# Kernel optimization log

Measured on AMD Instinct MI355X. Metric: run time of the kernel, lower is better.

## Reference

```python
import jax, jax.numpy as jnp
import numpy as np

_S = np.float32(1.0 / np.sqrt(2.0))
_lo = np.array([_S, _S], np.float32)   # dec_lo reversed == rec_lo for db1
_hi = np.array([_S, -_S], np.float32)  # dec_hi reversed == rec_hi for db1
# filters[k][i,j]: k=0 LL/2, k=1 hi(i)*lo(j), k=2 lo(i)*hi(j), k=3 hi*hi  (matches torch unsqueeze outer products)
DEC = np.stack([np.outer(_lo, _lo) / 2.0, np.outer(_hi, _lo), np.outer(_lo, _hi), np.outer(_hi, _hi)]).astype(np.float32)
INV = np.stack([np.outer(_lo, _lo) * 2.0, np.outer(_hi, _lo), np.outer(_lo, _hi), np.outer(_hi, _hi)]).astype(np.float32)
INV_FLIP = np.ascontiguousarray(INV[:, ::-1, ::-1])  # spatially flipped for conv_transpose-as-dilated-conv

DN = ('NCHW', 'OIHW', 'NCHW')


def wt(x):
    # single grouped (depthwise x4) strided conv == per-channel loop in the original
    N, C, H, W = x.shape
    k = jnp.broadcast_to(jnp.asarray(DEC)[None], (C, 4, 2, 2)).reshape(C * 4, 1, 2, 2)
    r = jax.lax.conv_general_dilated(x, k, (2, 2), 'VALID', dimension_numbers=DN, feature_group_count=C)
    r = r.reshape(N, C, 4, H // 2, W // 2)
    r = jnp.concatenate([r[:, :, :1], (r[:, :, 1:] + 1.0) / 2.0], axis=2)  # detail remap
    return r.reshape(N, 4 * C, H // 2, W // 2)


def iwt(v):
    N, C4, H, W = v.shape
    C = C4 // 4
    r = v.reshape(N, C, 4, H, W)
    r = jnp.concatenate([r[:, :, :1], 2.0 * r[:, :, 1:] - 1.0], axis=2).reshape(N, C4, H, W)
    k = jnp.broadcast_to(jnp.asarray(INV_FLIP)[None], (C, 4, 2, 2))
    # conv_transpose2d(stride=2, k=2) == dilated conv with lhs_dilation=2, pad 1, flipped kernel
    return jax.lax.conv_general_dilated(r, k, (1, 1), ((1, 1), (1, 1)), lhs_dilation=(2, 2),
                                        dimension_numbers=DN, feature_group_count=C)


def ws_conv(x, w, b, pad):
    # weight standardization: subtract mean over (in,kh,kw), divide by per-filter std (unbiased) + 1e-5
    wc = w - w.mean(axis=(1, 2, 3), keepdims=True)
    std = wc.reshape(w.shape[0], -1).std(axis=1, ddof=1).reshape(-1, 1, 1, 1) + 1e-5
    y = jax.lax.conv_general_dilated(x, wc / std, (1, 1), ((pad, pad), (pad, pad)), dimension_numbers=DN)
    return y if b is None else y + b[None, :, None, None]


def gn(x, g, b, G):
    N, C, H, W = x.shape
    xr = x.reshape(N, G, -1)
    m = xr.mean(-1, keepdims=True)
    v = xr.var(-1, keepdims=True)
    xr = (xr - m) * jax.lax.rsqrt(v + 1e-5)
    return xr.reshape(N, C, H, W) * g[None, :, None, None] + b[None, :, None, None]


def lrelu(t):
    return jnp.where(t > 0, t, 0.2 * t)


def setup_inputs() -> dict:
    key = jax.random.key(0)
    ks = iter(jax.random.split(key, 32))
    f32 = jnp.float32
    d = {}
    d['x'] = jax.random.normal(next(ks), (16, 3, 256, 256), f32)
    def wgt(shape):
        return 0.05 * jax.random.normal(next(ks), shape, f32)
    def bias(n):
        return 0.01 * jax.random.normal(next(ks), (n,), f32)
    c = 16
    d['conv1_w'], d['conv1_b'] = wgt((c, 12, 3, 3)), bias(c)
    d['conv2_w'], d['conv2_b'] = wgt((4 * c, 4 * c, 3, 3)), bias(4 * c)
    d['conv3_w'], d['conv3_b'] = wgt((16 * c, 16 * c, 3, 3)), bias(16 * c)
    d['conv4_w'], d['conv4_b'] = wgt((64 * c, 64 * c, 3, 3)), bias(64 * c)
    d['convd1_w'], d['convd1_b'] = wgt((12, c, 3, 3)), bias(12)
    d['convd2_w'], d['convd2_b'] = wgt((c, 2 * c, 3, 3)), bias(c)
    d['convd3_w'], d['convd3_b'] = wgt((4 * c, 8 * c, 3, 3)), bias(4 * c)
    d['convd4_w'], d['convd4_b'] = wgt((16 * c, 32 * c, 3, 3)), bias(16 * c)
    d['final_w'] = wgt((2, 3, 1, 1))
    for name, n in (('gn1', c), ('gn2', 4 * c), ('gn3', 16 * c), ('gn4', 64 * c)):
        d[name + '_w'] = 1.0 + 0.1 * jax.random.normal(next(ks), (n,), f32)
        d[name + '_b'] = 0.01 * jax.random.normal(next(ks), (n,), f32)
    return d


def reference(x, conv1_w, conv1_b, conv2_w, conv2_b, conv3_w, conv3_b, conv4_w, conv4_b,
              convd1_w, convd1_b, convd2_w, convd2_b, convd3_w, convd3_b, convd4_w, convd4_b,
              final_w, gn1_w, gn1_b, gn2_w, gn2_b, gn3_w, gn3_b, gn4_w, gn4_b):
    w1 = wt(x)
    c1 = gn(lrelu(ws_conv(w1, conv1_w, conv1_b, 1)), gn1_w, gn1_b, 2)
    w2 = wt(c1)
    c2 = gn(lrelu(ws_conv(w2, conv2_w, conv2_b, 1)), gn2_w, gn2_b, 8)
    w3 = wt(c2)
    c3 = gn(lrelu(ws_conv(w3, conv3_w, conv3_b, 1)), gn3_w, gn3_b, 32)
    w4 = wt(c3)
    c4 = gn(lrelu(ws_conv(w4, conv4_w, conv4_b, 1)), gn4_w, gn4_b, 128)
    c5 = gn(lrelu(ws_conv(c4, conv4_w, conv4_b, 1)), gn4_w, gn4_b, 128)
    c6 = ws_conv(c5, conv4_w, conv4_b, 1)
    ic4 = lrelu(c6 + w4)
    iw4 = jnp.concatenate([c3, iwt(ic4)], axis=1)
    ic3 = gn(lrelu(ws_conv(iw4, convd4_w, convd4_b, 1)), gn3_w, gn3_b, 32)
    iw3 = jnp.concatenate([c2, iwt(ic3)], axis=1)
    ic2 = gn(lrelu(ws_conv(iw3, convd3_w, convd3_b, 1)), gn2_w, gn2_b, 8)
    iw2 = jnp.concatenate([c1, iwt(ic2)], axis=1)
    ic1 = gn(lrelu(ws_conv(iw2, convd2_w, convd2_b, 1)), gn1_w, gn1_b, 2)
    iw1 = lrelu(ws_conv(ic1, convd1_w, convd1_b, 1))
    y = ws_conv(iwt(iw1), final_w, None, 0)
    return y
```

## Files before the change

kernel.cpp:

```cpp
#include <hip/hip_runtime.h>
#include <math.h>


#define NB 16

typedef _Float16 f16;
typedef _Float16 f16x8 __attribute__((ext_vector_type(8)));
typedef _Float16 f16x4 __attribute__((ext_vector_type(4)));
typedef float f32x4 __attribute__((ext_vector_type(4)));
typedef float f32x2 __attribute__((ext_vector_type(2)));
typedef unsigned int u32;

#define LLDS16(gp, lp)                                                          \
  __builtin_amdgcn_global_load_lds((const __attribute__((address_space(1))) u32*)(const void*)(gp), \
                                   (__attribute__((address_space(3))) u32*)(void*)(lp), 16, 0, 0)

__device__ __forceinline__ void ws_reduce(const float* wp, int fan, float* red,
                                          float& mean, float& inv) {
  float s = 0.f, s2 = 0.f;
  for (int i = threadIdx.x; i < fan; i += 256) { float v = wp[i]; s += v; s2 += v * v; }
  red[threadIdx.x] = s; red[256 + threadIdx.x] = s2;
  __syncthreads();
  for (int st = 128; st > 0; st >>= 1) {
    if (threadIdx.x < st) {
// ... 58 lines not shown

__global__ void halo2_kernel(f16* b0, int c0, int h0, int w0, int n0,
                             f16* b1, int c1, int h1, int w1, int total) {
  int idx = blockIdx.x * 256 + threadIdx.x;
  if (idx >= total) return;
  if (idx < n0) halo_write(b0, c0, h0, w0, idx);
  else halo_write(b1, c1, h1, w1, idx - n0);
}

__global__ void zero_halo_kernel(f16* __restrict__ buf, int C, int H, int W, int total8) {
  int idx = blockIdx.x * 256 + threadIdx.x;
  if (idx >= total8) return;
  halo_write(buf, C, H, W, idx);
}

__global__ void wt_kernel(const float* __restrict__ in, float* __restrict__ out,
                          int C, int Ho, int Wo, int total) {
  int idx = blockIdx.x * 256 + threadIdx.x;
  if (idx >= total) return;
  int w = idx % Wo; int t = idx / Wo;
  int h = t % Ho; t /= Ho;
  int c = t % C; int n = t / C;
  int Wi = 2 * Wo;
  const float* ip = in + (((size_t)n * C + c) * (2 * Ho) + 2 * h) * Wi + 2 * w;
  float a = ip[0], b = ip[1], cc = ip[Wi], d = ip[Wi + 1];
  size_t cs = (size_t)Ho * Wo;
  float* op = out + (((size_t)n * 4 * C + 4 * c) * Ho + h) * Wo + w;
  op[0]      = 0.25f * (a + b + cc + d);
  op[cs]     = 0.25f * (a + b - cc - d) + 0.5f;
  op[2 * cs] = 0.25f * (a - b + cc - d) + 0.5f;
  op[3 * cs] = 0.25f * (a - b - cc + d) + 0.5f;
}

__global__ __launch_bounds__(256) void wt_nhwc_kernel(
    const float* __restrict__ in, f16* __restrict__ out, float* __restrict__ out32,
    int C, int Ho, int Wo) {
  __shared__ f16 sm[32][264];
  int HWo = Ho * Wo;
  int p0 = blockIdx.x * 256, c0 = blockIdx.y * 8, n = blockIdx.z;
  int t = threadIdx.x;
  int p = p0 + t; int h = p / Wo; int ww = p - h * Wo;
  int Wi = 2 * Wo;
  int C4 = 4 * C;
#pragma unroll
  for (int r = 0; r < 8; ++r) {
    const float* ip = in + (((size_t)n * C + c0 + r) * (2 * Ho) + 2 * h) * Wi + 2 * ww;
    f32x2 u0 = *(const f32x2*)ip;
    f32x2 u1 = *(const f32x2*)(ip + Wi);
    float a = u0.x, b = u0.y, cc = u1.x, d = u1.y;
    float v0 = 0.25f * (a + b + cc + d);
    float v1 = 0.25f * (a + b - cc - d) + 0.5f;
    float v2 = 0.25f * (a - b + cc - d) + 0.5f;
    float v3 = 0.25f * (a - b - cc + d) + 0.5f;
    sm[4 * r][t]     = (f16)v0;
    sm[4 * r + 1][t] = (f16)v1;
    sm[4 * r + 2][t] = (f16)v2;
    sm[4 * r + 3][t] = (f16)v3;
    if (out32) {
      float* op = out32 + (((size_t)n * C4 + 4 * (c0 + r)) * Ho + h) * Wo + ww;
      size_t cs = (size_t)HWo;
      op[0] = v0; op[cs] = v1; op[2 * cs] = v2; op[3 * cs] = v3;
    }
  }
  __syncthreads();
#pragma unroll
  for (int i = 0; i < 4; ++i) {
    int c = t + i * 256;
    int pl = c >> 2, cio = (c & 3) * 8;
    f16x8 v;
#pragma unroll
    for (int u = 0; u < 8; ++u) v[u] = sm[cio + u][pl];
    int pp = p0 + pl; int y = pp / Wo; int x = pp - y * Wo;
    *(f16x8*)(out + (((size_t)n * (Ho + 2) + y + 1) * (Wo + 2) + x + 1) * C4 + c0 * 4 + cio) = v;
  }
}

__global__ void concat_iwt_kernel(const float* __restrict__ skip, const float* __restrict__ v,
                                  float* __restrict__ out, const float* __restrict__ gnp,
                                  const float* __restrict__ gamma, const float* __restrict__ beta,
                                  int G, int Sg, int len, int C, int Hh, int Wh,
                                  int totalA, int total) {
  int idx = blockIdx.x * 256 + threadIdx.x;
// ... 62 lines not shown
    f16* __restrict__ out, int C, int H, int W, int G, int Sg, int len) {
  __shared__ f16 sm[32][264];
  int HW = H * W;
  int p0 = blockIdx.x * 256, c0 = blockIdx.y * 32, n = blockIdx.z;
  int t = threadIdx.x;
  int cpg = C / G;
  const float* ip = in + ((size_t)n * C + c0) * HW + p0;
#pragma unroll 8
  for (int r = 0; r < 32; ++r) {
    int c = c0 + r; int g = c / cpg;
    const float* pp = gnp + (size_t)((n * G + g) * Sg) * 2;
    float s = 0.f, s2 = 0.f;
    for (int i = 0; i < Sg; ++i) { s += pp[2 * i]; s2 += pp[2 * i + 1]; }
    float mean = s / (float)len;
    float var = s2 / (float)len - mean * mean;
    if (var < 0.f) var = 0.f;
    float inv = rsqrtf(var + 1e-5f);
    float ga = gamma[c], be = beta[c];
    sm[r][t] = (f16)((ip[(size_t)r * HW + t] - mean) * inv * ga + be);
  }
  __syncthreads();
#pragma unroll
  for (int i = 0; i < 4; ++i) {
    int c = t + i * 256;
    int pl = c >> 2, cio = (c & 3) * 8;
    f16x8 v;
#pragma unroll
    for (int u = 0; u < 8; ++u) v[u] = sm[cio + u][pl];
    int p = p0 + pl; int y = p / W; int x = p - y * W;
    *(f16x8*)(out + (((size_t)n * (H + 2) + y + 1) * (W + 2) + x + 1) * C + c0 + cio) = v;
  }
}

__global__ __launch_bounds__(256) void conv_mfma6_kernel(
    const f16* __restrict__ A, const f16* __restrict__ Wp,
    f16* __restrict__ part, int Cin, int H, int W, int Cout, int HW) {
  constexpr int CH = 128 * 64;
  __shared__ f16 Asm[2 * CH];
  __shared__ f16 Bsm[2 * CH];

  const int tid = threadIdx.x;
  const int w = tid >> 6, lane = tid & 63;
  const int m0 = blockIdx.x * 128;
  const int co0 = blockIdx.y * 128;
  const int Wp2 = W + 2;

  const f16* gA[4]; const f16* gB[4];
  int lOff[4];
#pragma unroll
  for (int e = 0; e < 4; ++e) {
    int c = e * 256 + tid;
    int r = c >> 3, j = c & 7;
    int jx = j ^ (r & 7);
    int m = m0 + r; int n = m / HW; int p = m - n * HW;
    int y = p / W; int x = p - y * W;
    gA[e] = A + (((size_t)n * (H + 2) + y + 1) * Wp2 + (x + 1)) * Cin + jx * 8;
    gB[e] = Wp + (size_t)(co0 + r) * Cin + jx * 8;
    lOff[e] = (e * 256 + w * 64) * 8;
  }

  const int wm = w & 1, wn = w >> 1;
  const int lr = lane & 15, quad = lane >> 4;
  int aoffs[4][2], boffs[4][2];
#pragma unroll
  for (int i = 0; i < 4; ++i)
#pragma unroll
    for (int kk = 0; kk < 2; ++kk) {
      int r = wm * 64 + i * 16 + lr;
      int cidx = kk * 4 + quad;
      aoffs[i][kk] = (r * 8 + (cidx ^ (r & 7))) * 8;
      int rb = wn * 64 + i * 16 + lr;
      boffs[i][kk] = (rb * 8 + (cidx ^ (rb & 7))) * 8;
    }

  f32x4 acc[4][4];
#pragma unroll
  for (int i = 0; i < 4; ++i)
#pragma unroll
    for (int j = 0; j < 4; ++j) acc[i][j] = (f32x4){0.f, 0.f, 0.f, 0.f};

  const int kpt = Cin >> 6;
  const int nit = (9 * kpt) / gridDim.z;
  const int it0 = blockIdx.z * nit;
  const size_t bstride = (size_t)Cout * Cin;

  auto stageAB = [&](int it, int sel) {
    int tap = it / kpt, kk = it - tap * kpt;
    int dy = tap / 3 - 1, dx = tap % 3 - 1;
    long offA = ((long)dy * Wp2 + dx) * Cin + (kk << 6);
    long offB = (long)tap * bstride + (kk << 6);
    f16* ab = Asm + sel * CH;
    f16* bb = Bsm + sel * CH;
#pragma unroll
    for (int e = 0; e < 4; ++e) {
      LLDS16(gA[e] + offA, ab + lOff[e]);
      LLDS16(gB[e] + offB, bb + lOff[e]);
    }
  };

  stageAB(it0, 0);
  int sel = 0;
  for (int ii = 0; ii < nit; ++ii) {
    __syncthreads();
    if (ii + 1 < nit) stageAB(it0 + ii + 1, sel ^ 1);
    const f16* ab = Asm + sel * CH;
    const f16* bb = Bsm + sel * CH;
    f16x8 af[4][2], bf[4][2];
#pragma unroll
    for (int i = 0; i < 4; ++i)
#pragma unroll
      for (int kk = 0; kk < 2; ++kk) {
        af[i][kk] = *(const f16x8*)&ab[aoffs[i][kk]];
        bf[i][kk] = *(const f16x8*)&bb[boffs[i][kk]];
      }
#pragma unroll
    for (int kk = 0; kk < 2; ++kk)
#pragma unroll
      for (int i = 0; i < 4; ++i)
#pragma unroll
        for (int j = 0; j < 4; ++j)
          acc[i][j] = __builtin_amdgcn_mfma_f32_16x16x32_f16(af[i][kk], bf[j][kk], acc[i][j], 0, 0, 0);
    sel ^= 1;
  }

  const size_t pbase = (size_t)blockIdx.z * NB * Cout * HW;
#pragma unroll
  for (int i = 0; i < 4; ++i) {
    int mg = m0 + wm * 64 + i * 16 + quad * 4;
    int n = mg / HW, p = mg - n * HW;
#pragma unroll
    for (int j = 0; j < 4; ++j) {
      int co = co0 + wn * 64 + j * 16 + lr;
      f32x4 v = acc[i][j];
      f16x4 h;
#pragma unroll
      for (int r = 0; r < 4; ++r) h[r] = (f16)v[r];
      *(f16x4*)&part[pbase + ((size_t)n * Cout + co) * HW + p] = h;
    }
  }
}

__global__ __launch_bounds__(256) void reduceS_kernel(
    const f16* __restrict__ part, const float* __restrict__ bias,
    const float* __restrict__ add, float* __restrict__ out,
    int Cout, int HW, int S, int do_lrelu, int total4,
    float* __restrict__ gnp, int G, int Sg) {
  __shared__ float red[512];
  int idx = blockIdx.x * 256 + threadIdx.x;
  if (idx >= total4) return;
  size_t sstride = (size_t)NB * Cout * HW;
  int hw4 = HW >> 2;
  int p4 = idx % hw4; int t = idx / hw4;
  int c = t % Cout;
  size_t eoff = (size_t)t * HW + p4 * 4;
  float b = bias[c];
  f32x4 o = {b, b, b, b};
  for (int s = 0; s < S; ++s) {
    f16x4 a = *(const f16x4*)(part + s * sstride + eoff);
#pragma unroll
    for (int r = 0; r < 4; ++r) o[r] += (float)a[r];
  }
  if (add) {
    f32x4 av = *(const f32x4*)(add + eoff);
#pragma unroll
    for (int r = 0; r < 4; ++r) o[r] += av[r];
  }
  if (do_lrelu)
#pragma unroll
    for (int r = 0; r < 4; ++r) o[r] = o[r] > 0.f ? o[r] : 0.2f * o[r];
  *(f32x4*)(out + eoff) = o;
  if (gnp) {
    float ls = o[0] + o[1] + o[2] + o[3];
    float ls2 = o[0]*o[0] + o[1]*o[1] + o[2]*o[2] + o[3]*o[3];
    red[threadIdx.x] = ls; red[256 + threadIdx.x] = ls2;
    __syncthreads();
    for (int st = 128; st > 0; st >>= 1) {
      if (threadIdx.x < st) {
        red[threadIdx.x] += red[threadIdx.x + st];
        red[256 + threadIdx.x] += red[256 + threadIdx.x + st];
      }
      __syncthreads();
    }
    if (threadIdx.x == 0) {
      int flat0 = blockIdx.x * 1024;
      int chw = Cout * HW;
      int n = flat0 / chw;
      int rem = flat0 - n * chw;
      int L = (Cout / G) * HW;
      int g = rem / L;
      int s = (rem - g * L) >> 10;
      gnp[((n * G + g) * Sg + s) * 2] = red[0];
      gnp[((n * G + g) * Sg + s) * 2 + 1] = red[256];
    }
  }
}

__global__ __launch_bounds__(256) void conv_mfma3_kernel(
    const f16* __restrict__ A, const f16* __restrict__ Wp,
    const float* __restrict__ bias, float* __restrict__ out,
    int Cin, int H, int W, int Cout, int HW, int do_lrelu) {
  constexpr int CHA = 128 * 64;
  constexpr int CHB = 64 * 64;
  __shared__ f16 Asm[2 * CHA];
  __shared__ f16 Bsm[2 * CHB];

  const int tid = threadIdx.x;
  const int w = tid >> 6, lane = tid & 63;
  const int m0 = blockIdx.x * 128;
  const int co0 = blockIdx.y * 64;
  const int Wp2 = W + 2;

  const f16* gA[4];
  int lAoff[4];
#pragma unroll
  for (int e = 0; e < 4; ++e) {
    int c = e * 256 + tid;
    int r = c >> 3, j = c & 7;
    int jx = j ^ (r & 7);
    int m = m0 + r; int n = m / HW; int p = m - n * HW;
    int y = p / W; int x = p - y * W;
    gA[e] = A + (((size_t)n * (H + 2) + y + 1) * Wp2 + (x + 1)) * Cin + jx * 8;
    lAoff[e] = (e * 256 + w * 64) * 8;
  }
  const f16* gB[2];
  int lBoff[2];
// ... 160 lines not shown
    for (int co = 0; co < 8; ++co) { p0 += vout[co]; q0 += vout[co] * vout[co]; }
#pragma unroll
    for (int co = 8; co < CO; ++co) { p1 += vout[co]; q1 += vout[co] * vout[co]; }
    float* red = &sm[0][0][0];
    __syncthreads();
    red[tid] = p0; red[256 + tid] = q0; red[512 + tid] = p1; red[768 + tid] = q1;
    __syncthreads();
    for (int st = 128; st > 0; st >>= 1) {
      if (tid < st) {
        red[tid] += red[tid + st]; red[256 + tid] += red[256 + tid + st];
        red[512 + tid] += red[512 + tid + st]; red[768 + tid] += red[768 + tid + st];
      }
      __syncthreads();
    }
    if (tid == 0) {
      int S = gridDim.x;
      gnp[((n * 2 + 0) * S + blockIdx.x) * 2]     = red[0];
      gnp[((n * 2 + 0) * S + blockIdx.x) * 2 + 1] = red[256];
      gnp[((n * 2 + 1) * S + blockIdx.x) * 2]     = red[512];
      gnp[((n * 2 + 1) * S + blockIdx.x) * 2 + 1] = red[768];
    }
  }

  int oy = ty0 + ly, ox = tx0 + lx;
#pragma unroll
  for (int co = 0; co < CO; co++)
    out[(((size_t)n * Cout + co0 + co) * H + oy) * W + ox] = vout[co];
}

template <int CO, int CIC>
__global__ __launch_bounds__(256) void conv3x3_iwt_kernel(
    const float* __restrict__ in, const float* __restrict__ wgt,
    const float* __restrict__ bias, const float* __restrict__ fw,
    float* __restrict__ out, int Cin, int H, int W) {
  __shared__ float sm[CIC][18][18];
  int tiles_x = W >> 4;
  int bt = blockIdx.x;
  int tx0 = (bt % tiles_x) << 4;
  int ty0 = (bt / tiles_x) << 4;
  int n = blockIdx.z;
  int tid = threadIdx.x;
  int lx = tid & 15, ly = tid >> 4;

  float acc[CO];
#pragma unroll
  for (int i = 0; i < CO; i++) acc[i] = 0.f;

  const float* inb = in + (size_t)n * Cin * H * W;

  for (int ci0 = 0; ci0 < Cin; ci0 += CIC) {
    __syncthreads();
    for (int idx = tid; idx < CIC * 324; idx += 256) {
      int ci = idx / 324;
      int r = idx - ci * 324;
      int gy = r / 18, gx = r - gy * 18;
      int iy = ty0 + gy - 1, ix = tx0 + gx - 1;
      float v = 0.f;
      if ((unsigned)iy < (unsigned)H && (unsigned)ix < (unsigned)W)
        v = inb[((size_t)(ci0 + ci)) * H * W + (size_t)iy * W + ix];
      sm[ci][gy][gx] = v;
    }
    __syncthreads();
#pragma unroll
    for (int ci = 0; ci < CIC; ci++) {
      float x00 = sm[ci][ly][lx],     x01 = sm[ci][ly][lx + 1],     x02 = sm[ci][ly][lx + 2];
      float x10 = sm[ci][ly + 1][lx], x11 = sm[ci][ly + 1][lx + 1], x12 = sm[ci][ly + 1][lx + 2];
      float x20 = sm[ci][ly + 2][lx], x21 = sm[ci][ly + 2][lx + 1], x22 = sm[ci][ly + 2][lx + 2];
      const float* wp = wgt + (size_t)(ci0 + ci) * 9;
#pragma unroll
      for (int co = 0; co < CO; co++) {
        const float* wc = wp + (size_t)co * Cin * 9;
        float a = acc[co];
        a = fmaf(wc[0], x00, a); a = fmaf(wc[1], x01, a); a = fmaf(wc[2], x02, a);
        a = fmaf(wc[3], x10, a); a = fmaf(wc[4], x11, a); a = fmaf(wc[5], x12, a);
        a = fmaf(wc[6], x20, a); a = fmaf(wc[7], x21, a); a = fmaf(wc[8], x22, a);
        acc[co] = a;
      }
    }
  }

  float vout[CO];
#pragma unroll
  for (int co = 0; co < CO; co++) {
    float v = acc[co] + bias[co];
    vout[co] = v > 0.f ? v : 0.2f * v;
  }

  float y0[3], y1[3], y2[3], y3[3];
#pragma unroll
  for (int c = 0; c < 3; ++c) {
    float v0 = vout[4 * c];
    float v1 = 2.f * vout[4 * c + 1] - 1.f;
// ... 22 lines not shown

__global__ __launch_bounds__(256) void gn_stats_kernel(const float* __restrict__ x,
                                                       float* __restrict__ part,
                                                       int C, int HW, int G, int SPLIT) {
  __shared__ float red[512];
  int gs = blockIdx.x;
  int g = gs / SPLIT, s = gs - g * SPLIT;
  int n = blockIdx.y;
  int cpg = C / G;
  int len = cpg * HW;
  int chunk = len / SPLIT;
  size_t base = ((size_t)n * C + (size_t)g * cpg) * HW + (size_t)s * chunk;
  const f32x4* xp = (const f32x4*)(x + base);
  int chunk4 = chunk >> 2;
  float sm = 0.f, s2 = 0.f;
  for (int i = threadIdx.x; i < chunk4; i += 256) {
    f32x4 v = xp[i];
    sm += v.x + v.y + v.z + v.w;
    s2 += v.x * v.x + v.y * v.y + v.z * v.z + v.w * v.w;
  }
  red[threadIdx.x] = sm; red[256 + threadIdx.x] = s2;
  __syncthreads();
  for (int st = 128; st > 0; st >>= 1) {
    if (threadIdx.x < st) {
      red[threadIdx.x] += red[threadIdx.x + st];
      red[256 + threadIdx.x] += red[256 + threadIdx.x + st];
    }
    __syncthreads();
  }
  if (threadIdx.x == 0) {
    int o = ((n * G + g) * SPLIT + s) * 2;
    part[o] = red[0]; part[o + 1] = red[256];
  }
}

__global__ __launch_bounds__(256) void gn_apply_kernel(float* __restrict__ x,
                                                       const float* __restrict__ gnp,
                                                       const float* __restrict__ gamma,
                                                       const float* __restrict__ beta,
                                                       int C, int HW, int G, int Sg, int len,
                                                       int total4) {
  int idx = blockIdx.x * 256 + threadIdx.x;
  if (idx >= total4) return;
  int flat0 = blockIdx.x * 1024;
  int chw = C * HW;
  int n = flat0 / chw;
  int rem = flat0 - n * chw;
  int L = (C / G) * HW;
  int g = rem / L;
  const float* pp = gnp + (size_t)((n * G + g) * Sg) * 2;
  float s = 0.f, s2 = 0.f;
  for (int i = 0; i < Sg; ++i) { s += pp[2 * i]; s2 += pp[2 * i + 1]; }
  float mean = s / (float)len;
  float var = s2 / (float)len - mean * mean;
  if (var < 0.f) var = 0.f;
  float inv = rsqrtf(var + 1e-5f);
  int hw4 = HW >> 2;
  int p4 = idx % hw4; int t = idx / hw4;
  int c = t % C;
  float ga = gamma[c], be = beta[c];
  f32x4* xp = (f32x4*)(x + ((size_t)t * HW)) + p4;
  f32x4 v = *xp;
#pragma unroll
  for (int r = 0; r < 4; ++r) v[r] = (v[r] - mean) * inv * ga + be;
  *xp = v;
}


extern "C" void kernel_launch(void* const* d_in, const int* in_sizes, int n_in,
                              void* d_out, int out_size, void* d_ws, size_t ws_size,
                              hipStream_t stream) {
  const float* x        = (const float*)d_in[0];
  const float* conv1_w  = (const float*)d_in[1];
  const float* conv1_b  = (const float*)d_in[2];
  const float* conv2_w  = (const float*)d_in[3];
  const float* conv2_b  = (const float*)d_in[4];
  const float* conv3_w  = (const float*)d_in[5];
  const float* conv3_b  = (const float*)d_in[6];
  const float* conv4_w  = (const float*)d_in[7];
  const float* conv4_b  = (const float*)d_in[8];
  const float* convd1_w = (const float*)d_in[9];
  const float* convd1_b = (const float*)d_in[10];
  const float* convd2_w = (const float*)d_in[11];
  const float* convd2_b = (const float*)d_in[12];
  const float* convd3_w = (const float*)d_in[13];
  const float* convd3_b = (const float*)d_in[14];
  const float* convd4_w = (const float*)d_in[15];
  const float* convd4_b = (const float*)d_in[16];
  const float* final_w  = (const float*)d_in[17];
  const float* gn1_w = (const float*)d_in[18];
  const float* gn1_b = (const float*)d_in[19];
  const float* gn2_w = (const float*)d_in[20];
  const float* gn2_b = (const float*)d_in[21];
  const float* gn3_w = (const float*)d_in[22];
  const float* gn3_b = (const float*)d_in[23];
  const float* gn4_w = (const float*)d_in[24];
  const float* gn4_b = (const float*)d_in[25];

  char* base = (char*)d_ws;
  size_t off = 0;
  auto allocB = [&](size_t bytes) { size_t o = off; off = (off + bytes + 255) & ~(size_t)255; return o; };

  size_t o_sw1  = allocB(16 * 108 * 4);
  size_t o_swd1 = allocB(12 * 144 * 4);
  size_t o_swd2 = allocB(16 * 288 * 4);
  size_t o_swf  = allocB(6 * 4);
  size_t o_pw2  = allocB((size_t)9 * 64 * 64 * 2);
  size_t o_pw3  = allocB((size_t)9 * 256 * 256 * 2);
  size_t o_pw4  = allocB((size_t)9 * 1024 * 1024 * 2);
  size_t o_pwd3 = allocB((size_t)9 * 64 * 128 * 2);
  size_t o_pwd4 = allocB((size_t)9 * 256 * 512 * 2);
  size_t o_R1   = allocB((size_t)NB * 66 * 66 * 128 * 2);
  size_t o_R2   = allocB((size_t)NB * 34 * 34 * 512 * 2);
  size_t o_gnp  = allocB(16384 * 4);
  size_t o_c1 = allocB((size_t)NB * 16 * 128 * 128 * 4);
  size_t o_c2 = allocB((size_t)NB * 64 * 64 * 64 * 4);
  size_t o_c3 = allocB((size_t)NB * 256 * 32 * 32 * 4);
  size_t o_w4 = allocB((size_t)NB * 1024 * 16 * 16 * 4);
  size_t o_t1 = allocB((size_t)NB * 1024 * 16 * 16 * 4);
  size_t o_t2 = allocB((size_t)NB * 512 * 32 * 32 * 4);

  if (off > ws_size) return;

  float* c1 = (float*)(base + o_c1);
  float* c2 = (float*)(base + o_c2);
  float* c3 = (float*)(base + o_c3);
  float* w4 = (float*)(base + o_w4);
  float* t1 = (float*)(base + o_t1);
  float* t2 = (float*)(base + o_t2);
  f16* part  = (f16*)(base + o_R1);
  f16* ah64  = (f16*)(base + o_R1);
  f16* ah128 = (f16*)(base + o_R1);
  f16* ah256 = (f16*)(base + o_R2);
  f16* ah1k  = (f16*)(base + o_R2);
  f16* ah512 = (f16*)(base + o_R2);
  f16* pw2 = (f16*)(base + o_pw2);
  f16* pw3 = (f16*)(base + o_pw3);
  f16* pw4 = (f16*)(base + o_pw4);
  f16* pwd3 = (f16*)(base + o_pwd3);
  f16* pwd4 = (f16*)(base + o_pwd4);
  float* gnp = (float*)(base + o_gnp);

  {
    int n0 = NB * (2 * 66 + 2 * 64) * (64 / 8);
    int n1 = NB * (2 * 34 + 2 * 32) * (256 / 8);
    int tot = n0 + n1;
    halo2_kernel<<<(tot + 255) / 256, 256, 0, stream>>>(ah64, 64, 64, 64, n0,
                                                        ah256, 256, 32, 32, tot);
  }
  ws_all_kernel<<<46, 256, 0, stream>>>(conv1_w, (float*)(base + o_sw1),
                                        convd1_w, (float*)(base + o_swd1),
                                        convd2_w, (float*)(base + o_swd2),
                                        final_w, (float*)(base + o_swf));
  ws_f16_all_kernel<<<1664, 256, 0, stream>>>(conv2_w, pw2, conv3_w, pw3, conv4_w, pw4,
                                              convd3_w, pwd3, convd4_w, pwd4);

  auto prep_nhwc = [&](const float* in, f16* ah, int C, int H, int W, int zero) {
    if (zero) {
      int total8 = NB * (2 * (W + 2) + 2 * H) * (C / 8);
      zero_halo_kernel<<<(total8 + 255) / 256, 256, 0, stream>>>(ah, C, H, W, total8);
    }
    dim3 g((H * W) / 256, C / 32, NB);
    to_nhwc_pad_kernel<<<g, 256, 0, stream>>>(in, ah, C, H, W);
  };
  auto wt_nhwc = [&](const float* in, f16* ah, float* copy32, int C, int Ho, int Wo) {
    dim3 g((Ho * Wo) / 256, C / 8, NB);
    wt_nhwc_kernel<<<g, 256, 0, stream>>>(in, ah, copy32, C, Ho, Wo);
  };
  auto cm6 = [&](const f16* a, const f16* wt, const float* b, float* dest, const float* add,
                 int Cin, int Hs, int Ws, int Cout, int lr, int G, int Sg) {
    dim3 g((NB * Hs * Ws) / 128, Cout / 128, 2);
    conv_mfma6_kernel<<<g, 256, 0, stream>>>(a, wt, part, Cin, Hs, Ws, Cout, Hs * Ws);
    int total4 = (NB * Cout * Hs * Ws) >> 2;
    reduceS_kernel<<<(total4 + 255) / 256, 256, 0, stream>>>(
        part, b, add, dest, Cout, Hs * Ws, 2, lr, total4, G ? gnp : nullptr, G, Sg);
  };
  auto cm3 = [&](const f16* a, const f16* wt, const float* b, float* o,
                 int Cin, int Hs, int Ws, int Cout, int lr) {
    dim3 g((NB * Hs * Ws) / 128, Cout / 64);
    conv_mfma3_kernel<<<g, 256, 0, stream>>>(a, wt, b, o, Cin, Hs, Ws, Cout, Hs * Ws, lr);
  };
  auto apply = [&](float* xb, const float* g, const float* b, int C, int HW, int G, int Sg) {
    int len = (C / G) * HW;
    int total4 = (NB * C * HW) >> 2;
    gn_apply_kernel<<<(total4 + 255) / 256, 256, 0, stream>>>(xb, gnp, g, b, C, HW, G, Sg,
                                                              len, total4);
  };
  auto stats = [&](const float* xb, int C, int HW, int G, int SPLIT) {
    dim3 gsd(G * SPLIT, NB);
    gn_stats_kernel<<<gsd, 256, 0, stream>>>(xb, gnp, C, HW, G, SPLIT);
  };
  auto concat_iwt = [&](const float* skip, const float* v, float* out, int C, int Hh, int Wh,
                        const float* gg, const float* gb, int G, int Sg) {
    int totalA = NB * C * 4 * Hh * Wh;
    int total = totalA + NB * C * Hh * Wh;
    int len = G ? ((4 * C) / G) * Hh * Wh : 1;
    concat_iwt_kernel<<<(total + 255) / 256, 256, 0, stream>>>(
        skip, v, out, G ? gnp : nullptr, gg, gb, G, Sg, len, C, Hh, Wh, totalA, total);
  };

  {
    int total = NB * 3 * 128 * 128;
    wt_kernel<<<(total + 255) / 256, 256, 0, stream>>>(x, t1, 3, 128, 128, total);
  }
  {
    dim3 g(64, 1, NB);
    conv3x3_kernel<16, 4><<<g, 256, 0, stream>>>(t1, (float*)(base + o_sw1), conv1_b,
                                                 c1, 12, 128, 128, 16, 1, gnp);
  }
  apply(c1, gn1_w, gn1_b, 16, 128 * 128, 2, 64);

  wt_nhwc(c1, ah64, nullptr, 16, 64, 64);
  cm3(ah64, pw2, conv2_b, c2, 64, 64, 64, 64, 1);
  stats(c2, 64, 4096, 8, 16);
  apply(c2, gn2_w, gn2_b, 64, 4096, 8, 16);

  wt_nhwc(c2, ah256, nullptr, 64, 32, 32);
  cm6(ah256, pw3, conv3_b, c3, nullptr, 256, 32, 32, 256, 1, 32, 8);
  apply(c3, gn3_w, gn3_b, 256, 1024, 32, 8);

  {
    int total8 = NB * (2 * 18 + 2 * 16) * (1024 / 8);
    zero_halo_kernel<<<(total8 + 255) / 256, 256, 0, stream>>>(ah1k, 1024, 16, 16, total8);
  }
  wt_nhwc(c3, ah1k, w4, 256, 16, 16);

  cm6(ah1k, pw4, conv4_b, t1, nullptr, 1024, 16, 16, 1024, 1, 128, 2);
  {
    dim3 g(1, 32, NB);
    gn_nhwc_kernel<<<g, 256, 0, stream>>>(t1, gnp, gn4_w, gn4_b, ah1k, 1024, 16, 16,
                                          128, 2, 2048);
  }
  cm6(ah1k, pw4, conv4_b, t2, nullptr, 1024, 16, 16, 1024, 1, 128, 2);
  {
    dim3 g(1, 32, NB);
    gn_nhwc_kernel<<<g, 256, 0, stream>>>(t2, gnp, gn4_w, gn4_b, ah1k, 1024, 16, 16,
                                          128, 2, 2048);
  }
  cm6(ah1k, pw4, conv4_b, t1, w4, 1024, 16, 16, 1024, 1, 0, 0);

  concat_iwt(c3, t1, t2, 256, 16, 16, nullptr, nullptr, 0, 0);
  prep_nhwc(t2, ah512, 512, 32, 32, 1);
  cm6(ah512, pwd4, convd4_b, t1, nullptr, 512, 32, 32, 256, 1, 32, 8);
  concat_iwt(c2, t1, t2, 64, 32, 32, gn3_w, gn3_b, 32, 8);
  prep_nhwc(t2, ah128, 128, 64, 64, 1);
  cm3(ah128, pwd3, convd3_b, t1, 128, 64, 64, 64, 1);
  stats(t1, 64, 4096, 8, 16);
  concat_iwt(c1, t1, t2, 16, 64, 64, gn2_w, gn2_b, 8, 16);
  {
    dim3 g(64, 1, NB);
    conv3x3_kernel<16, 4><<<g, 256, 0, stream>>>(t2, (float*)(base + o_swd2), convd2_b,
                                                 t1, 32, 128, 128, 16, 1, gnp);
  }
  apply(t1, gn1_w, gn1_b, 16, 128 * 128, 2, 64);
  {
    dim3 g(64, 1, NB);
    conv3x3_iwt_kernel<12, 4><<<g, 256, 0, stream>>>(t1, (float*)(base + o_swd1), convd1_b,
                                                     (float*)(base + o_swf), (float*)d_out,
                                                     16, 128, 128);
  }
}
```

Before: 921.5 us.

## Replace split-K conv plus reduce pass with fused 64x128 MFMA conv epilogue

Replaces the split-K (z=2) 128x128 MFMA conv, which wrote fp16 partials that a separate reduce kernel summed, with a 64x128-tile kernel that runs the full K loop. The new kernel applies bias, residual add and leaky ReLU in its epilogue and computes GroupNorm partial sums with wave shuffles. This removes the partial-buffer round trip and one launch per conv, and the smaller M tile keeps the block count up without splitting K. In exchange, each block runs twice as many K iterations, B-tile reuse per block drops, and the GN split count changes to HW/64.

```diff
diff --git a/kernel.cpp b/kernel.cpp
--- a/kernel.cpp
+++ b/kernel.cpp
@@ -258,56 +258,72 @@
   }
 }
 
-__global__ __launch_bounds__(256) void conv_mfma6_kernel(
+__global__ __launch_bounds__(256) void conv_mfma5_kernel(
     const f16* __restrict__ A, const f16* __restrict__ Wp,
-    f16* __restrict__ part, int Cin, int H, int W, int Cout, int HW) {
-  constexpr int CH = 128 * 64;
-  __shared__ f16 Asm[2 * CH];
-  __shared__ f16 Bsm[2 * CH];
+    const float* __restrict__ bias, const float* __restrict__ add,
+    float* __restrict__ out, int Cin, int H, int W, int Cout, int HW,
+    int do_lrelu, float* __restrict__ gnp, int G) {
+  constexpr int CHA = 64 * 64;
+  constexpr int CHB = 128 * 64;
+  __shared__ f16 Asm[2 * CHA];
+  __shared__ f16 Bsm[2 * CHB];
+  __shared__ float redg[64];
 
   const int tid = threadIdx.x;
   const int w = tid >> 6, lane = tid & 63;
-  const int m0 = blockIdx.x * 128;
+  const int m0 = blockIdx.x * 64;
   const int co0 = blockIdx.y * 128;
   const int Wp2 = W + 2;
 
-  const f16* gA[4]; const f16* gB[4];
-  int lOff[4];
-#pragma unroll
-  for (int e = 0; e < 4; ++e) {
+  const f16* gA[2]; int lAoff[2];
+#pragma unroll
+  for (int e = 0; e < 2; ++e) {
     int c = e * 256 + tid;
     int r = c >> 3, j = c & 7;
     int jx = j ^ (r & 7);
     int m = m0 + r; int n = m / HW; int p = m - n * HW;
     int y = p / W; int x = p - y * W;
     gA[e] = A + (((size_t)n * (H + 2) + y + 1) * Wp2 + (x + 1)) * Cin + jx * 8;
+    lAoff[e] = (e * 256 + w * 64) * 8;
+  }
+  const f16* gB[4]; int lBoff[4];
+#pragma unroll
+  for (int e = 0; e < 4; ++e) {
+    int c = e * 256 + tid;
+    int r = c >> 3, j = c & 7;
+    int jx = j ^ (r & 7);
     gB[e] = Wp + (size_t)(co0 + r) * Cin + jx * 8;
-    lOff[e] = (e * 256 + w * 64) * 8;
+    lBoff[e] = (e * 256 + w * 64) * 8;
   }
 
   const int wm = w & 1, wn = w >> 1;
   const int lr = lane & 15, quad = lane >> 4;
-  int aoffs[4][2], boffs[4][2];
-#pragma unroll
-  for (int i = 0; i < 4; ++i)
+  int aoffs[2][2], boffs[4][2];
+#pragma unroll
+  for (int i = 0; i < 2; ++i)
 #pragma unroll
     for (int kk = 0; kk < 2; ++kk) {
-      int r = wm * 64 + i * 16 + lr;
+      int r = wm * 32 + i * 16 + lr;
       int cidx = kk * 4 + quad;
       aoffs[i][kk] = (r * 8 + (cidx ^ (r & 7))) * 8;
-      int rb = wn * 64 + i * 16 + lr;
-      boffs[i][kk] = (rb * 8 + (cidx ^ (rb & 7))) * 8;
-    }
-
-  f32x4 acc[4][4];
-#pragma unroll
-  for (int i = 0; i < 4; ++i)
+    }
+#pragma unroll
+  for (int j = 0; j < 4; ++j)
+#pragma unroll
+    for (int kk = 0; kk < 2; ++kk) {
+      int rb = wn * 64 + j * 16 + lr;
+      int cidx = kk * 4 + quad;
+      boffs[j][kk] = (rb * 8 + (cidx ^ (rb & 7))) * 8;
+    }
+
+  f32x4 acc[2][4];
+#pragma unroll
+  for (int i = 0; i < 2; ++i)
 #pragma unroll
     for (int j = 0; j < 4; ++j) acc[i][j] = (f32x4){0.f, 0.f, 0.f, 0.f};
 
   const int kpt = Cin >> 6;
-  const int nit = (9 * kpt) / gridDim.z;
-  const int it0 = blockIdx.z * nit;
+  const int nit = 9 * kpt;
   const size_t bstride = (size_t)Cout * Cin;
 
   auto stageAB = [&](int it, int sel) {
@@ -315,108 +331,94 @@
     int dy = tap / 3 - 1, dx = tap % 3 - 1;
     long offA = ((long)dy * Wp2 + dx) * Cin + (kk << 6);
     long offB = (long)tap * bstride + (kk << 6);
-    f16* ab = Asm + sel * CH;
-    f16* bb = Bsm + sel * CH;
-#pragma unroll
-    for (int e = 0; e < 4; ++e) {
-      LLDS16(gA[e] + offA, ab + lOff[e]);
-      LLDS16(gB[e] + offB, bb + lOff[e]);
-    }
+    f16* ab = Asm + sel * CHA;
+    f16* bb = Bsm + sel * CHB;
+#pragma unroll
+    for (int e = 0; e < 2; ++e) LLDS16(gA[e] + offA, ab + lAoff[e]);
+#pragma unroll
+    for (int e = 0; e < 4; ++e) LLDS16(gB[e] + offB, bb + lBoff[e]);
   };
 
-  stageAB(it0, 0);
+  stageAB(0, 0);
   int sel = 0;
   for (int ii = 0; ii < nit; ++ii) {
     __syncthreads();
-    if (ii + 1 < nit) stageAB(it0 + ii + 1, sel ^ 1);
-    const f16* ab = Asm + sel * CH;
-    const f16* bb = Bsm + sel * CH;
-    f16x8 af[4][2], bf[4][2];
-#pragma unroll
-    for (int i = 0; i < 4; ++i)
-#pragma unroll
-      for (int kk = 0; kk < 2; ++kk) {
-        af[i][kk] = *(const f16x8*)&ab[aoffs[i][kk]];
-        bf[i][kk] = *(const f16x8*)&bb[boffs[i][kk]];
-      }
+    if (ii + 1 < nit) stageAB(ii + 1, sel ^ 1);
+    const f16* ab = Asm + sel * CHA;
+    const f16* bb = Bsm + sel * CHB;
+    f16x8 af[2][2], bf[4][2];
+#pragma unroll
+    for (int i = 0; i < 2; ++i)
+#pragma unroll
+      for (int kk = 0; kk < 2; ++kk) af[i][kk] = *(const f16x8*)&ab[aoffs[i][kk]];
+#pragma unroll
+    for (int j = 0; j < 4; ++j)
+#pragma unroll
+      for (int kk = 0; kk < 2; ++kk) bf[j][kk] = *(const f16x8*)&bb[boffs[j][kk]];
 #pragma unroll
     for (int kk = 0; kk < 2; ++kk)
 #pragma unroll
-      for (int i = 0; i < 4; ++i)
+      for (int i = 0; i < 2; ++i)
 #pragma unroll
         for (int j = 0; j < 4; ++j)
           acc[i][j] = __builtin_amdgcn_mfma_f32_16x16x32_f16(af[i][kk], bf[j][kk], acc[i][j], 0, 0, 0);
     sel ^= 1;
   }
 
-  const size_t pbase = (size_t)blockIdx.z * NB * Cout * HW;
-#pragma unroll
-  for (int i = 0; i < 4; ++i) {
-    int mg = m0 + wm * 64 + i * 16 + quad * 4;
+  float lsj[4] = {0.f, 0.f, 0.f, 0.f}, ls2j[4] = {0.f, 0.f, 0.f, 0.f};
+#pragma unroll
+  for (int i = 0; i < 2; ++i) {
+    int mg = m0 + wm * 32 + i * 16 + quad * 4;
     int n = mg / HW, p = mg - n * HW;
 #pragma unroll
     for (int j = 0; j < 4; ++j) {
       int co = co0 + wn * 64 + j * 16 + lr;
+      float b = bias[co];
       f32x4 v = acc[i][j];
-      f16x4 h;
-#pragma unroll
-      for (int r = 0; r < 4; ++r) h[r] = (f16)v[r];
-      *(f16x4*)&part[pbase + ((size_t)n * Cout + co) * HW + p] = h;
-    }
-  }
-}
-
-__global__ __launch_bounds__(256) void reduceS_kernel(
-    const f16* __restrict__ part, const float* __restrict__ bias,
-    const float* __restrict__ add, float* __restrict__ out,
-    int Cout, int HW, int S, int do_lrelu, int total4,
-    float* __restrict__ gnp, int G, int Sg) {
-  __shared__ float red[512];
-  int idx = blockIdx.x * 256 + threadIdx.x;
-  if (idx >= total4) return;
-  size_t sstride = (size_t)NB * Cout * HW;
-  int hw4 = HW >> 2;
-  int p4 = idx % hw4; int t = idx / hw4;
-  int c = t % Cout;
-  size_t eoff = (size_t)t * HW + p4 * 4;
-  float b = bias[c];
-  f32x4 o = {b, b, b, b};
-  for (int s = 0; s < S; ++s) {
-    f16x4 a = *(const f16x4*)(part + s * sstride + eoff);
-#pragma unroll
-    for (int r = 0; r < 4; ++r) o[r] += (float)a[r];
-  }
-  if (add) {
-    f32x4 av = *(const f32x4*)(add + eoff);
-#pragma unroll
-    for (int r = 0; r < 4; ++r) o[r] += av[r];
-  }
-  if (do_lrelu)
-#pragma unroll
-    for (int r = 0; r < 4; ++r) o[r] = o[r] > 0.f ? o[r] : 0.2f * o[r];
-  *(f32x4*)(out + eoff) = o;
+      size_t eoff = ((size_t)n * Cout + co) * HW + p;
+      if (add) {
+        f32x4 av = *(const f32x4*)(add + eoff);
+#pragma unroll
+        for (int r = 0; r < 4; ++r) v[r] += av[r];
+      }
+#pragma unroll
+      for (int r = 0; r < 4; ++r) {
+        float u = v[r] + b;
+        u = (do_lrelu && u < 0.f) ? 0.2f * u : u;
+        v[r] = u;
+        lsj[j] += u; ls2j[j] += u * u;
+      }
+      *(f32x4*)&out[eoff] = v;
+    }
+  }
+
   if (gnp) {
-    float ls = o[0] + o[1] + o[2] + o[3];
-    float ls2 = o[0]*o[0] + o[1]*o[1] + o[2]*o[2] + o[3]*o[3];
-    red[threadIdx.x] = ls; red[256 + threadIdx.x] = ls2;
-    __syncthreads();
-    for (int st = 128; st > 0; st >>= 1) {
-      if (threadIdx.x < st) {
-        red[threadIdx.x] += red[threadIdx.x + st];
-        red[256 + threadIdx.x] += red[256 + threadIdx.x + st];
+    __syncthreads();
+#pragma unroll
+    for (int j = 0; j < 4; ++j) {
+      float s = lsj[j], s2 = ls2j[j];
+      s += __shfl_xor(s, 1);  s2 += __shfl_xor(s2, 1);
+      s += __shfl_xor(s, 2);  s2 += __shfl_xor(s2, 2);
+      s += __shfl_xor(s, 4);  s2 += __shfl_xor(s2, 4);
+      s += __shfl_xor(s, 16); s2 += __shfl_xor(s2, 16);
+      s += __shfl_xor(s, 32); s2 += __shfl_xor(s2, 32);
+      if ((lane & 55) == 0) {
+        int hi = (lane >> 3) & 1;
+        int g = wn * 8 + j * 2 + hi;
+        redg[(g * 2 + wm) * 2]     = s;
+        redg[(g * 2 + wm) * 2 + 1] = s2;
       }
-      __syncthreads();
-    }
-    if (threadIdx.x == 0) {
-      int flat0 = blockIdx.x * 1024;
-      int chw = Cout * HW;
-      int n = flat0 / chw;
-      int rem = flat0 - n * chw;
-      int L = (Cout / G) * HW;
-      int g = rem / L;
-      int s = (rem - g * L) >> 10;
-      gnp[((n * G + g) * Sg + s) * 2] = red[0];
-      gnp[((n * G + g) * Sg + s) * 2 + 1] = red[256];
+    }
+    __syncthreads();
+    if (tid < 16) {
+      float s  = redg[(tid * 2) * 2]     + redg[(tid * 2 + 1) * 2];
+      float s2 = redg[(tid * 2) * 2 + 1] + redg[(tid * 2 + 1) * 2 + 1];
+      int n = m0 / HW;
+      int sidx = (m0 - n * HW) >> 6;
+      int Sg = HW >> 6;
+      int gg = (co0 >> 3) + tid;
+      gnp[((n * G + gg) * Sg + sidx) * 2]     = s;
+      gnp[((n * G + gg) * Sg + sidx) * 2 + 1] = s2;
     }
   }
 }
@@ -853,7 +855,6 @@
   float* w4 = (float*)(base + o_w4);
   float* t1 = (float*)(base + o_t1);
   float* t2 = (float*)(base + o_t2);
-  f16* part  = (f16*)(base + o_R1);
   f16* ah64  = (f16*)(base + o_R1);
   f16* ah128 = (f16*)(base + o_R1);
   f16* ah256 = (f16*)(base + o_R2);
@@ -892,13 +893,11 @@
     dim3 g((Ho * Wo) / 256, C / 8, NB);
     wt_nhwc_kernel<<<g, 256, 0, stream>>>(in, ah, copy32, C, Ho, Wo);
   };
-  auto cm6 = [&](const f16* a, const f16* wt, const float* b, float* dest, const float* add,
-                 int Cin, int Hs, int Ws, int Cout, int lr, int G, int Sg) {
-    dim3 g((NB * Hs * Ws) / 128, Cout / 128, 2);
-    conv_mfma6_kernel<<<g, 256, 0, stream>>>(a, wt, part, Cin, Hs, Ws, Cout, Hs * Ws);
-    int total4 = (NB * Cout * Hs * Ws) >> 2;
-    reduceS_kernel<<<(total4 + 255) / 256, 256, 0, stream>>>(
-        part, b, add, dest, Cout, Hs * Ws, 2, lr, total4, G ? gnp : nullptr, G, Sg);
+  auto cm5 = [&](const f16* a, const f16* wt, const float* b, float* dest, const float* add,
+                 int Cin, int Hs, int Ws, int Cout, int lr, float* gp, int G) {
+    dim3 g((NB * Hs * Ws) / 64, Cout / 128);
+    conv_mfma5_kernel<<<g, 256, 0, stream>>>(a, wt, b, add, dest, Cin, Hs, Ws, Cout,
+                                             Hs * Ws, lr, gp, G);
   };
   auto cm3 = [&](const f16* a, const f16* wt, const float* b, float* o,
                  int Cin, int Hs, int Ws, int Cout, int lr) {
@@ -941,8 +940,8 @@
   apply(c2, gn2_w, gn2_b, 64, 4096, 8, 16);
 
   wt_nhwc(c2, ah256, nullptr, 64, 32, 32);
-  cm6(ah256, pw3, conv3_b, c3, nullptr, 256, 32, 32, 256, 1, 32, 8);
-  apply(c3, gn3_w, gn3_b, 256, 1024, 32, 8);
+  cm5(ah256, pw3, conv3_b, c3, nullptr, 256, 32, 32, 256, 1, gnp, 32);
+  apply(c3, gn3_w, gn3_b, 256, 1024, 32, 16);
 
   {
     int total8 = NB * (2 * 18 + 2 * 16) * (1024 / 8);
@@ -950,24 +949,24 @@
   }
   wt_nhwc(c3, ah1k, w4, 256, 16, 16);
 
-  cm6(ah1k, pw4, conv4_b, t1, nullptr, 1024, 16, 16, 1024, 1, 128, 2);
+  cm5(ah1k, pw4, conv4_b, t1, nullptr, 1024, 16, 16, 1024, 1, gnp, 128);
   {
     dim3 g(1, 32, NB);
     gn_nhwc_kernel<<<g, 256, 0, stream>>>(t1, gnp, gn4_w, gn4_b, ah1k, 1024, 16, 16,
-                                          128, 2, 2048);
-  }
-  cm6(ah1k, pw4, conv4_b, t2, nullptr, 1024, 16, 16, 1024, 1, 128, 2);
+                                          128, 4, 2048);
+  }
+  cm5(ah1k, pw4, conv4_b, t2, nullptr, 1024, 16, 16, 1024, 1, gnp, 128);
   {
     dim3 g(1, 32, NB);
     gn_nhwc_kernel<<<g, 256, 0, stream>>>(t2, gnp, gn4_w, gn4_b, ah1k, 1024, 16, 16,
-                                          128, 2, 2048);
-  }
-  cm6(ah1k, pw4, conv4_b, t1, w4, 1024, 16, 16, 1024, 1, 0, 0);
+                                          128, 4, 2048);
+  }
+  cm5(ah1k, pw4, conv4_b, t1, w4, 1024, 16, 16, 1024, 1, nullptr, 0);
 
   concat_iwt(c3, t1, t2, 256, 16, 16, nullptr, nullptr, 0, 0);
   prep_nhwc(t2, ah512, 512, 32, 32, 1);
-  cm6(ah512, pwd4, convd4_b, t1, nullptr, 512, 32, 32, 256, 1, 32, 8);
-  concat_iwt(c2, t1, t2, 64, 32, 32, gn3_w, gn3_b, 32, 8);
+  cm5(ah512, pwd4, convd4_b, t1, nullptr, 512, 32, 32, 256, 1, gnp, 32);
+  concat_iwt(c2, t1, t2, 64, 32, 32, gn3_w, gn3_b, 32, 16);
   prep_nhwc(t2, ah128, 128, 64, 64, 1);
   cm3(ah128, pwd3, convd3_b, t1, 128, 64, 64, 64, 1);
   stats(t1, 64, 4096, 8, 16);
```

New measurement: 1.016 ms. +10.2%, slower.

## Fuse GroupNorm apply into Haar transform and final conv loaders

Applied to the files above, without the earlier changes.

Removes the standalone gn_apply_kernel passes. Group-norm scale and shift are now computed per channel inside the wavelet NHWC kernel and inside the final conv3x3_iwt tile loader, and applied on the fly. Where the normalized tensor is still needed later as a skip connection (c1, c2, c3), the wavelet kernel writes the normalized values back in place. This saves one read pass per GN stage and one full read-write pass for the last GN, at the cost of a small per-block stats reduction and a normalize step during loads.

```diff
diff --git a/kernel.cpp b/kernel.cpp
--- a/kernel.cpp
+++ b/kernel.cpp
@@ -114,22 +114,49 @@
   op[3 * cs] = 0.25f * (a - b - cc + d) + 0.5f;
 }
 
-__global__ __launch_bounds__(256) void wt_nhwc_kernel(
-    const float* __restrict__ in, f16* __restrict__ out, float* __restrict__ out32,
+__global__ __launch_bounds__(256) void wt_nhwc_gn_kernel(
+    const float* __restrict__ in, const float* __restrict__ gnp,
+    const float* __restrict__ gamma, const float* __restrict__ beta,
+    int G, int Sg, int len,
+    f16* __restrict__ out, float* __restrict__ out32, float* __restrict__ gnwb,
     int C, int Ho, int Wo) {
   __shared__ f16 sm[32][264];
+  __shared__ float scs[8], shs[8];
   int HWo = Ho * Wo;
   int p0 = blockIdx.x * 256, c0 = blockIdx.y * 8, n = blockIdx.z;
   int t = threadIdx.x;
+  if (t < 8) {
+    int c = c0 + t;
+    int g = c / (C / G);
+    const float* pp = gnp + (size_t)((n * G + g) * Sg) * 2;
+    float s = 0.f, s2 = 0.f;
+    for (int i = 0; i < Sg; ++i) { s += pp[2 * i]; s2 += pp[2 * i + 1]; }
+    float mean = s / (float)len;
+    float var = s2 / (float)len - mean * mean;
+    if (var < 0.f) var = 0.f;
+    float inv = rsqrtf(var + 1e-5f);
+    float ga = gamma[c];
+    scs[t] = inv * ga;
+    shs[t] = beta[c] - mean * inv * ga;
+  }
+  __syncthreads();
   int p = p0 + t; int h = p / Wo; int ww = p - h * Wo;
   int Wi = 2 * Wo;
   int C4 = 4 * C;
 #pragma unroll
   for (int r = 0; r < 8; ++r) {
-    const float* ip = in + (((size_t)n * C + c0 + r) * (2 * Ho) + 2 * h) * Wi + 2 * ww;
+    size_t ioff = (((size_t)n * C + c0 + r) * (2 * Ho) + 2 * h) * Wi + 2 * ww;
+    const float* ip = in + ioff;
     f32x2 u0 = *(const f32x2*)ip;
     f32x2 u1 = *(const f32x2*)(ip + Wi);
-    float a = u0.x, b = u0.y, cc = u1.x, d = u1.y;
+    float sc = scs[r], sh = shs[r];
+    float a = u0.x * sc + sh, b = u0.y * sc + sh;
+    float cc = u1.x * sc + sh, d = u1.y * sc + sh;
+    if (gnwb) {
+      float* wp = gnwb + ioff;
+      *(f32x2*)wp = (f32x2){a, b};
+      *(f32x2*)(wp + Wi) = (f32x2){cc, d};
+    }
     float v0 = 0.25f * (a + b + cc + d);
     float v1 = 0.25f * (a + b - cc - d) + 0.5f;
     float v2 = 0.25f * (a - b + cc - d) + 0.5f;
@@ -643,8 +670,11 @@
 __global__ __launch_bounds__(256) void conv3x3_iwt_kernel(
     const float* __restrict__ in, const float* __restrict__ wgt,
     const float* __restrict__ bias, const float* __restrict__ fw,
+    const float* __restrict__ gnp, const float* __restrict__ gamma,
+    const float* __restrict__ beta, int G, int Sg, int len,
     float* __restrict__ out, int Cin, int H, int W) {
   __shared__ float sm[CIC][18][18];
+  __shared__ float csc[16], csh[16];
   int tiles_x = W >> 4;
   int bt = blockIdx.x;
   int tx0 = (bt % tiles_x) << 4;
@@ -653,6 +683,21 @@
   int tid = threadIdx.x;
   int lx = tid & 15, ly = tid >> 4;
 
+  if (tid < Cin) {
+    int g = tid / (Cin / G);
+    const float* pp = gnp + (size_t)((n * G + g) * Sg) * 2;
+    float s = 0.f, s2 = 0.f;
+    for (int i = 0; i < Sg; ++i) { s += pp[2 * i]; s2 += pp[2 * i + 1]; }
+    float mean = s / (float)len;
+    float var = s2 / (float)len - mean * mean;
+    if (var < 0.f) var = 0.f;
+    float inv = rsqrtf(var + 1e-5f);
+    float ga = gamma[tid];
+    csc[tid] = inv * ga;
+    csh[tid] = beta[tid] - mean * inv * ga;
+  }
+  __syncthreads();
+
   float acc[CO];
 #pragma unroll
   for (int i = 0; i < CO; i++) acc[i] = 0.f;
@@ -668,7 +713,7 @@
       int iy = ty0 + gy - 1, ix = tx0 + gx - 1;
       float v = 0.f;
       if ((unsigned)iy < (unsigned)H && (unsigned)ix < (unsigned)W)
-        v = inb[((size_t)(ci0 + ci)) * H * W + (size_t)iy * W + ix];
+        v = inb[((size_t)(ci0 + ci)) * H * W + (size_t)iy * W + ix] * csc[ci0 + ci] + csh[ci0 + ci];
       sm[ci][gy][gx] = v;
     }
     __syncthreads();
@@ -757,38 +802,6 @@
     int o = ((n * G + g) * SPLIT + s) * 2;
     part[o] = red[0]; part[o + 1] = red[256];
   }
-}
-
-__global__ __launch_bounds__(256) void gn_apply_kernel(float* __restrict__ x,
-                                                       const float* __restrict__ gnp,
-                                                       const float* __restrict__ gamma,
-                                                       const float* __restrict__ beta,
-                                                       int C, int HW, int G, int Sg, int len,
-                                                       int total4) {
-  int idx = blockIdx.x * 256 + threadIdx.x;
-  if (idx >= total4) return;
-  int flat0 = blockIdx.x * 1024;
-  int chw = C * HW;
-  int n = flat0 / chw;
-  int rem = flat0 - n * chw;
-  int L = (C / G) * HW;
-  int g = rem / L;
-  const float* pp = gnp + (size_t)((n * G + g) * Sg) * 2;
-  float s = 0.f, s2 = 0.f;
-  for (int i = 0; i < Sg; ++i) { s += pp[2 * i]; s2 += pp[2 * i + 1]; }
-  float mean = s / (float)len;
-  float var = s2 / (float)len - mean * mean;
-  if (var < 0.f) var = 0.f;
-  float inv = rsqrtf(var + 1e-5f);
-  int hw4 = HW >> 2;
-  int p4 = idx % hw4; int t = idx / hw4;
-  int c = t % C;
-  float ga = gamma[c], be = beta[c];
-  f32x4* xp = (f32x4*)(x + ((size_t)t * HW)) + p4;
-  f32x4 v = *xp;
-#pragma unroll
-  for (int r = 0; r < 4; ++r) v[r] = (v[r] - mean) * inv * ga + be;
-  *xp = v;
 }
 
 
@@ -888,9 +901,13 @@
     dim3 g((H * W) / 256, C / 32, NB);
     to_nhwc_pad_kernel<<<g, 256, 0, stream>>>(in, ah, C, H, W);
   };
-  auto wt_nhwc = [&](const float* in, f16* ah, float* copy32, int C, int Ho, int Wo) {
+  auto wt_nhwc_gn = [&](const float* in, f16* ah, float* haar32, float* wb,
+                        const float* gg, const float* gb, int G, int Sg,
+                        int C, int Ho, int Wo) {
+    int len = (C / G) * (4 * Ho * Wo);
     dim3 g((Ho * Wo) / 256, C / 8, NB);
-    wt_nhwc_kernel<<<g, 256, 0, stream>>>(in, ah, copy32, C, Ho, Wo);
+    wt_nhwc_gn_kernel<<<g, 256, 0, stream>>>(in, gnp, gg, gb, G, Sg, len,
+                                             ah, haar32, wb, C, Ho, Wo);
   };
   auto cm6 = [&](const f16* a, const f16* wt, const float* b, float* dest, const float* add,
                  int Cin, int Hs, int Ws, int Cout, int lr, int G, int Sg) {
@@ -905,12 +922,6 @@
     dim3 g((NB * Hs * Ws) / 128, Cout / 64);
     conv_mfma3_kernel<<<g, 256, 0, stream>>>(a, wt, b, o, Cin, Hs, Ws, Cout, Hs * Ws, lr);
   };
-  auto apply = [&](float* xb, const float* g, const float* b, int C, int HW, int G, int Sg) {
-    int len = (C / G) * HW;
-    int total4 = (NB * C * HW) >> 2;
-    gn_apply_kernel<<<(total4 + 255) / 256, 256, 0, stream>>>(xb, gnp, g, b, C, HW, G, Sg,
-                                                              len, total4);
-  };
   auto stats = [&](const float* xb, int C, int HW, int G, int SPLIT) {
     dim3 gsd(G * SPLIT, NB);
     gn_stats_kernel<<<gsd, 256, 0, stream>>>(xb, gnp, C, HW, G, SPLIT);
@@ -933,22 +944,18 @@
     conv3x3_kernel<16, 4><<<g, 256, 0, stream>>>(t1, (float*)(base + o_sw1), conv1_b,
                                                  c1, 12, 128, 128, 16, 1, gnp);
   }
-  apply(c1, gn1_w, gn1_b, 16, 128 * 128, 2, 64);
-
-  wt_nhwc(c1, ah64, nullptr, 16, 64, 64);
+  wt_nhwc_gn(c1, ah64, nullptr, c1, gn1_w, gn1_b, 2, 64, 16, 64, 64);
+
   cm3(ah64, pw2, conv2_b, c2, 64, 64, 64, 64, 1);
   stats(c2, 64, 4096, 8, 16);
-  apply(c2, gn2_w, gn2_b, 64, 4096, 8, 16);
-
-  wt_nhwc(c2, ah256, nullptr, 64, 32, 32);
+  wt_nhwc_gn(c2, ah256, nullptr, c2, gn2_w, gn2_b, 8, 16, 64, 32, 32);
+
   cm6(ah256, pw3, conv3_b, c3, nullptr, 256, 32, 32, 256, 1, 32, 8);
-  apply(c3, gn3_w, gn3_b, 256, 1024, 32, 8);
-
   {
     int total8 = NB * (2 * 18 + 2 * 16) * (1024 / 8);
     zero_halo_kernel<<<(total8 + 255) / 256, 256, 0, stream>>>(ah1k, 1024, 16, 16, total8);
   }
-  wt_nhwc(c3, ah1k, w4, 256, 16, 16);
+  wt_nhwc_gn(c3, ah1k, w4, c3, gn3_w, gn3_b, 32, 8, 256, 16, 16);
 
   cm6(ah1k, pw4, conv4_b, t1, nullptr, 1024, 16, 16, 1024, 1, 128, 2);
   {
@@ -977,11 +984,10 @@
     conv3x3_kernel<16, 4><<<g, 256, 0, stream>>>(t2, (float*)(base + o_swd2), convd2_b,
                                                  t1, 32, 128, 128, 16, 1, gnp);
   }
-  apply(t1, gn1_w, gn1_b, 16, 128 * 128, 2, 64);
   {
     dim3 g(64, 1, NB);
-    conv3x3_iwt_kernel<12, 4><<<g, 256, 0, stream>>>(t1, (float*)(base + o_swd1), convd1_b,
-                                                     (float*)(base + o_swf), (float*)d_out,
-                                                     16, 128, 128);
-  }
-}
+    conv3x3_iwt_kernel<12, 4><<<g, 256, 0, stream>>>(
+        t1, (float*)(base + o_swd1), convd1_b, (float*)(base + o_swf),
+        gnp, gn1_w, gn1_b, 2, 64, 8 * 128 * 128, (float*)d_out, 16, 128, 128);
+  }
+}
```

Result: faster. 887.5 us (-3.7%).
